# Performance work log

Hardware: AMD Instinct MI355X
Metric: run time of the kernel (lower is better)

The kernel has to match this reference:

```python
import jax, jax.numpy as jnp
import numpy as np

B, S, DM = 1, 2048, 2048
H, KV, DH = 32, 8, 64
ROT, DQ = 32, 16  # rotary dims; DQ = ROT // 2
GROUPS = H // KV


def setup_inputs() -> dict:
    key = jax.random.key(0)
    ks = jax.random.split(key, 9)
    sc = 0.02
    hidden_states = jax.random.normal(ks[0], (B, S, DM), jnp.float32)
    # realistic RoPE tables: theta = pos * inv_freq, shape [1,1,S,DQ] (broadcasts over heads)
    inv_freq = 1.0 / (10000.0 ** (jnp.arange(DQ, dtype=jnp.float32) / DQ))
    ang = jnp.arange(S, dtype=jnp.float32)[:, None] * inv_freq[None, :]
    cos = jnp.cos(ang)[None, None]
    sin = jnp.sin(ang)[None, None]
    position_ids = jnp.broadcast_to(jnp.arange(S, dtype=jnp.int64 if jax.config.read('jax_enable_x64') else jnp.int32), (B, S))
    Wq = jax.random.normal(ks[1], (DM, H * DH), jnp.float32) * sc
    Wk = jax.random.normal(ks[2], (DM, KV * DH), jnp.float32) * sc
    Wv = jax.random.normal(ks[3], (DM, KV * DH), jnp.float32) * sc
    Wo = jax.random.normal(ks[4], (H * DH, DM), jnp.float32) * sc
    qkv_dim = H * DH + 2 * KV * DH
    tau_Wq = jax.random.normal(ks[5], (qkv_dim, H), jnp.float32) * sc
    tau_Wv = jax.random.normal(ks[6], (qkv_dim, H), jnp.float32) * sc
    tau_alpha = jax.random.normal(ks[7], (H,), jnp.float32)
    return {"hidden_states": hidden_states, "cos": cos, "sin": sin,
            "position_ids": position_ids, "Wq": Wq, "Wk": Wk, "Wv": Wv,
            "Wo": Wo, "tau_Wq": tau_Wq, "tau_Wv": tau_Wv, "tau_alpha": tau_alpha}


def _rope(x, cos, sin):
    # x: [B, h, S, DH]; rotate first ROT dims (half-split real/imag), interleave output
    x_rot, x_pass = x[..., :ROT], x[..., ROT:]
    xr, xi = x_rot[..., :DQ], x_rot[..., DQ:]
    out_r = xr * cos - xi * sin
    out_i = xr * sin + xi * cos
    out = jnp.stack([out_r, out_i], axis=-1).reshape(x.shape[:-1] + (ROT,))
    return jnp.concatenate([out, x_pass], axis=-1)


def reference(hidden_states, cos, sin, position_ids, Wq, Wk, Wv, Wo, tau_Wq, tau_Wv, tau_alpha):
    b, s, _ = hidden_states.shape
    q = hidden_states @ Wq                      # [B,S,H*DH]
    k = hidden_states @ Wk                      # [B,S,KV*DH]
    v = hidden_states @ Wv                      # [B,S,KV*DH]
    # tau gating: gelu(concat qkv) -> tanh projections -> position sigmoid term
    feat = jax.nn.gelu(jnp.concatenate([q, k, v], axis=-1), approximate=False)
    tok_q = jnp.tanh(feat @ tau_Wq).transpose(0, 2, 1)   # [B,H,S]
    tok_v = jnp.tanh(feat @ tau_Wv).transpose(0, 2, 1)   # [B,H,S]
    pos = position_ids.astype(hidden_states.dtype) + 1.0
    tau_pos = 1.0 + (jax.nn.sigmoid(tau_alpha[None, :, None] * jnp.log(pos)[:, None, :]) - 0.5)
    tau_q = (tok_q + tau_pos)[..., None]        # [B,H,S,1]
    tau_v = (tok_v + tau_pos)[..., None]        # [B,H,S,1]
    q = q.reshape(b, s, H, DH).transpose(0, 2, 1, 3) * tau_q   # [B,H,S,DH]
    k = k.reshape(b, s, KV, DH).transpose(0, 2, 1, 3)          # [B,KV,S,DH]
    # torch: tau_v.repeat(1,groups,1,1)[:, :KV] == first KV heads of tau_v
    v = v.reshape(b, s, KV, DH).transpose(0, 2, 1, 3) * tau_v[:, :KV]
    q = _rope(q, cos, sin)
    k = _rope(k, cos, sin)
    # GQA expand kv heads, causal SDPA
    k = jnp.repeat(k, GROUPS, axis=1)
    v = jnp.repeat(v, GROUPS, axis=1)
    scores = jnp.einsum('bhqd,bhkd->bhqk', q, k) / np.sqrt(DH).astype(np.float32)
    causal = jnp.tril(jnp.ones((s, s), dtype=bool))
    scores = jnp.where(causal, scores, jnp.finfo(scores.dtype).min)
    attn = jax.nn.softmax(scores, axis=-1)
    out = jnp.einsum('bhqk,bhkd->bhqd', attn, v)
    out = out.transpose(0, 2, 1, 3).reshape(b, s, H * DH)
    return out @ Wo
```

## Files before the change

kernel.cpp:

```cpp
#include <hip/hip_runtime.h>
#include <cmath>

typedef __bf16 bf16x8 __attribute__((ext_vector_type(8)));
typedef __bf16 bf16x4 __attribute__((ext_vector_type(4)));
typedef float f32x4 __attribute__((ext_vector_type(4)));
typedef short s16x4 __attribute__((ext_vector_type(4)));
typedef unsigned short u16;
typedef unsigned int u32;

__device__ __forceinline__ u16 f2bf(float f) {
  union { float f; unsigned int u; } v; v.f = f;
  unsigned int u = v.u;
  return (u16)((u + 0x7FFFu + ((u >> 16) & 1u)) >> 16);
}

__device__ __forceinline__ float bf2f(u16 b) {
  union { u32 u; float f; } v; v.u = (u32)b << 16; return v.f;
}

__device__ __forceinline__ float geluf(float x) {
  return 0.5f * x * (1.0f + erff(x * 0.7071067811865475f));
}

__device__ __forceinline__ f32x4 mfma_16x16x16_bf16(s16x4 a, s16x4 b, f32x4 c) {
#if __has_builtin(__builtin_amdgcn_mfma_f32_16x16x16bf16_1k)
  return __builtin_amdgcn_mfma_f32_16x16x16bf16_1k(a, b, c, 0, 0, 0);
#else
  f32x4 d;
  asm volatile("v_mfma_f32_16x16x16_bf16 %0, %1, %2, %3"
               : "=v"(d) : "v"(a), "v"(b), "0"(c));
  return d;
#endif
}

__device__ __forceinline__ void gl_lds16(const void* g, void* l) {
  __builtin_amdgcn_global_load_lds(
      (const __attribute__((address_space(1))) u32*)g,
      (__attribute__((address_space(3))) u32*)l, 16, 0, 0);
}

__global__ __launch_bounds__(256) void cvt_bf16(const float* __restrict__ in,
                                                u16* __restrict__ out, int n8) {
  int i = blockIdx.x * 256 + threadIdx.x;
  if (i >= n8) return;
  const float4* p = (const float4*)in + 2 * (size_t)i;
  float4 a = p[0], b = p[1];
  uint4 o;
  o.x = (unsigned)f2bf(a.x) | ((unsigned)f2bf(a.y) << 16);
  o.y = (unsigned)f2bf(a.z) | ((unsigned)f2bf(a.w) << 16);
  o.z = (unsigned)f2bf(b.x) | ((unsigned)f2bf(b.y) << 16);
  o.w = (unsigned)f2bf(b.z) | ((unsigned)f2bf(b.w) << 16);
  ((uint4*)out)[i] = o;
}

__global__ __launch_bounds__(256) void transpose_all(const float* __restrict__ Wq,
                                                     const float* __restrict__ Wk,
                                                     const float* __restrict__ Wv,
                                                     const float* __restrict__ Wo,
                                                     const float* __restrict__ tWq,
                                                     const float* __restrict__ tWv,
                                                     u16* __restrict__ WqkvT,
                                                     u16* __restrict__ WoT,
                                                     u16* __restrict__ Tt) {
  __shared__ float tile[64][65];
  int b = blockIdx.x;
  const float* in; u16* out; int R, C, bx, by;
  if (b < 1024)      { in = Wq;  out = WqkvT;                R = 2048; C = 2048; bx = b & 31; by = b >> 5; }
  else if (b < 1280) { b -= 1024; in = Wk; out = WqkvT + 2048ull * 2048; R = 2048; C = 512; bx = b & 7; by = b >> 3; }
  else if (b < 1536) { b -= 1280; in = Wv; out = WqkvT + 2560ull * 2048; R = 2048; C = 512; bx = b & 7; by = b >> 3; }
  else if (b < 2560) { b -= 1536; in = Wo; out = WoT;        R = 2048; C = 2048; bx = b & 31; by = b >> 5; }
  else if (b < 2608) { b -= 2560; in = tWq; out = Tt;               R = 3072; C = 32; bx = 0; by = b; }
  else               { b -= 2608; in = tWv; out = Tt + 32ull * 3072; R = 3072; C = 32; bx = 0; by = b; }

  const int t = threadIdx.x;
  const int r0 = by * 64, c0 = bx * 64;
  const int lr = t >> 4, lc4 = (t & 15) * 4;
#pragma unroll
  for (int p = 0; p < 4; ++p) {
    int r = p * 16 + lr;
    float4 v = {0.f, 0.f, 0.f, 0.f};
    if (c0 + lc4 < C) v = *(const float4*)(in + (size_t)(r0 + r) * C + c0 + lc4);
    tile[r][lc4] = v.x; tile[r][lc4 + 1] = v.y;
    tile[r][lc4 + 2] = v.z; tile[r][lc4 + 3] = v.w;
  }
  __syncthreads();
  const int cg = t >> 4, rr4 = (t & 15) * 4;
#pragma unroll
  for (int p = 0; p < 4; ++p) {
    int c = p * 16 + cg;
    if (c0 + c < C) {
      uint2 w;
      w.x = (u32)f2bf(tile[rr4][c])     | ((u32)f2bf(tile[rr4 + 1][c]) << 16);
      w.y = (u32)f2bf(tile[rr4 + 2][c]) | ((u32)f2bf(tile[rr4 + 3][c]) << 16);
      *(uint2*)(out + (size_t)(c0 + c) * R + r0 + rr4) = w;
    }
  }
}

template <int WR, int WC>
__global__ __launch_bounds__(256, 3) void gemm_bt(const u16* __restrict__ A,
                                                  const u16* __restrict__ Bt,
                                                  float* __restrict__ Cpart,
                                                  int M, int N, int K, int kPer) {
  constexpr int BM = WR * 64, BN = WC * 64;
  __shared__ __attribute__((aligned(16))) u16 As[BM * 64];
  __shared__ __attribute__((aligned(16))) u16 Bs[BN * 64];
  const int tid = threadIdx.x, wid = tid >> 6, lane = tid & 63;
  const int l16 = lane & 15, quad = lane >> 4;
  const int wm = (wid % WR) * 64, wn = (wid / WR) * 64;
  const int m0 = blockIdx.y * BM, n0 = blockIdx.x * BN;
  const int kIters = K >> 6;
  const int kStart = blockIdx.z * kPer;
  const int kEnd = (kStart + kPer < kIters) ? (kStart + kPer) : kIters;

  const int lrow = lane >> 3;
  const int swz = (lane & 7) ^ lrow;
  const u16* gAb = A + (size_t)m0 * K + (size_t)swz * 8;
  const u16* gBb = Bt + (size_t)n0 * K + (size_t)swz * 8;
  const int sx = l16 & 7;

  f32x4 acc[4][4] = {};
  for (int kt = kStart; kt < kEnd; ++kt) {
    __syncthreads();
    const u16* gA = gAb + (size_t)kt * 64;
    const u16* gB = gBb + (size_t)kt * 64;
#pragma unroll
    for (int j = 0; j < BM / 32; ++j) {
      int i = wid * (BM / 32) + j;
      gl_lds16(gA + (size_t)(i * 8 + lrow) * K, &As[i * 512]);
    }
#pragma unroll
    for (int j = 0; j < BN / 32; ++j) {
      int i = wid * (BN / 32) + j;
      gl_lds16(gB + (size_t)(i * 8 + lrow) * K, &Bs[i * 512]);
    }
    __syncthreads();
    bf16x8 af[4][2], bfr[4][2];
#pragma unroll
    for (int mt = 0; mt < 4; ++mt)
#pragma unroll
      for (int ks = 0; ks < 2; ++ks)
        af[mt][ks] = *(const bf16x8*)(&As[(wm + mt * 16 + l16) * 64 +
                                          (((ks * 4 + quad) ^ sx) * 8)]);
#pragma unroll
    for (int nt = 0; nt < 4; ++nt)
#pragma unroll
      for (int ks = 0; ks < 2; ++ks)
        bfr[nt][ks] = *(const bf16x8*)(&Bs[(wn + nt * 16 + l16) * 64 +
                                           (((ks * 4 + quad) ^ sx) * 8)]);
#pragma unroll
    for (int mt = 0; mt < 4; ++mt)
#pragma unroll
      for (int nt = 0; nt < 4; ++nt)
#pragma unroll
        for (int ks = 0; ks < 2; ++ks)
          acc[mt][nt] = __builtin_amdgcn_mfma_f32_16x16x32_bf16(
              af[mt][ks], bfr[nt][ks], acc[mt][nt], 0, 0, 0);
  }

  float* C = Cpart + (size_t)blockIdx.z * M * N;
#pragma unroll
  for (int mt = 0; mt < 4; ++mt)
#pragma unroll
    for (int nt = 0; nt < 4; ++nt)
#pragma unroll
      for (int r = 0; r < 4; ++r) {
        int row = m0 + wm + mt * 16 + quad * 4 + r;
        int col = n0 + wn + nt * 16 + l16;
        C[(size_t)row * N + col] = acc[mt][nt][r];
      }
}

__global__ __launch_bounds__(256) void reduce_gelu(float* __restrict__ base, int P,
                                                   int n4, u16* __restrict__ gout) {
  int i = blockIdx.x * 256 + threadIdx.x;
  if (i >= n4) return;
  size_t n = (size_t)n4 * 4;
  float4 v = ((const float4*)base)[i];
  for (int p = 1; p < P; ++p) {
    float4 w = ((const float4*)(base + (size_t)p * n))[i];
    v.x += w.x; v.y += w.y; v.z += w.z; v.w += w.w;
  }
  if (P > 1) ((float4*)base)[i] = v;
  uint2 o;
  o.x = (u32)f2bf(geluf(v.x)) | ((u32)f2bf(geluf(v.y)) << 16);
  o.y = (u32)f2bf(geluf(v.z)) | ((u32)f2bf(geluf(v.w)) << 16);
  ((uint2*)gout)[i] = o;
}

__global__ __launch_bounds__(256) void reduce_add(const float* __restrict__ base, int P,
                                                  int n4, float* __restrict__ dst) {
  int i = blockIdx.x * 256 + threadIdx.x;
  if (i >= n4) return;
  size_t n = (size_t)n4 * 4;
  float4 v = ((const float4*)base)[i];
  for (int p = 1; p < P; ++p) {
    float4 w = ((const float4*)(base + (size_t)p * n))[i];
    v.x += w.x; v.y += w.y; v.z += w.z; v.w += w.w;
  }
  ((float4*)dst)[i] = v;
}

__global__ __launch_bounds__(256) void reduce_tanh(const float* __restrict__ base, int P,
                                                   int n, float* __restrict__ tokq,
                                                   float* __restrict__ tokv) {
  int i = blockIdx.x * 256 + threadIdx.x;
  if (i >= n) return;
  float v = base[i];
  for (int p = 1; p < P; ++p) v += base[(size_t)p * n + i];
  float t = tanhf(v);
  int col = i & 63, row = i >> 6;
  if (col < 32) tokq[row * 32 + col] = t;
  else          tokv[row * 32 + (col - 32)] = t;
}

#define QSCALE 0.18033688011112042f
__global__ __launch_bounds__(256) void prep_qkv(const float* __restrict__ qkv,
                                                const float* __restrict__ tokq,
                                                const float* __restrict__ tokv,
                                                const float* __restrict__ alpha,
                                                const float* __restrict__ cosb,
                                                const float* __restrict__ sinb,
                                                const int* __restrict__ pos_ids,
                                                u16* __restrict__ Qb,
                                                u16* __restrict__ Kb,
                                                u16* __restrict__ Vt,
                                                u16* __restrict__ Vb) {
  const int s = blockIdx.x;
  const int tid = threadIdx.x;
  __shared__ float cs[16], sn[16], tq_s[32], tv_s[32];
  if (tid < 16) { cs[tid] = cosb[s * 16 + tid]; sn[tid] = sinb[s * 16 + tid]; }
  if (tid < 32) {
    float p = (float)pos_ids[s] + 1.0f;
    float sig = 1.0f / (1.0f + __expf(-alpha[tid] * logf(p)));
    float taupos = 0.5f + sig;
    tq_s[tid] = (tokq[s * 32 + tid] + taupos) * QSCALE;
    tv_s[tid] = tokv[s * 32 + tid] + taupos;
  }
  __syncthreads();
  const float* row = qkv + (size_t)s * 3072;

  for (int idx = tid; idx < 2048; idx += 256) {
    int h = idx >> 6, d = idx & 63;
    float tq = tq_s[h];
    float v;
    if (d < 32) {
      int i = d >> 1;
      float xr = row[h * 64 + i] * tq, xi = row[h * 64 + 16 + i] * tq;
      v = (d & 1) ? (xr * sn[i] + xi * cs[i]) : (xr * cs[i] - xi * sn[i]);
    } else v = row[h * 64 + d] * tq;
    Qb[((size_t)h * 2048 + s) * 64 + d] = f2bf(v);
  }
  for (int idx = tid; idx < 512; idx += 256) {
    int h = idx >> 6, d = idx & 63;
    const float* kr = row + 2048;
    float v;
    if (d < 32) {
      int i = d >> 1;
      float xr = kr[h * 64 + i], xi = kr[h * 64 + 16 + i];
      v = (d & 1) ? (xr * sn[i] + xi * cs[i]) : (xr * cs[i] - xi * sn[i]);
    } else v = kr[h * 64 + d];
    Kb[((size_t)h * 2048 + s) * 64 + d] = f2bf(v);
  }
  for (int idx = tid; idx < 512; idx += 256) {
    int h = idx >> 6, d = idx & 63;
    float v = row[2560 + h * 64 + d] * tv_s[h];
    u16 b = f2bf(v);
    if (Vb) Vb[((size_t)h * 2048 + s) * 64 + d] = b;
    else    Vt[((size_t)h * 64 + d) * 2048 + s] = b;
  }
}

__global__ __launch_bounds__(256) void vtrans(const u16* __restrict__ Vb,
                                              u16* __restrict__ Vt) {
  __shared__ u16 t[64][68];
  const int s0 = blockIdx.x * 64, h = blockIdx.y;
  const int tid = threadIdx.x;
  const u16* src = Vb + ((size_t)h * 2048 + s0) * 64;
#pragma unroll
  for (int p = 0; p < 4; ++p) {
    int v = p * 256 + tid;
    int r = v >> 4, c = (v & 15) * 4;
    uint2 w = *(const uint2*)(src + (size_t)r * 64 + c);
    t[r][c] = (u16)(w.x & 0xffff); t[r][c + 1] = (u16)(w.x >> 16);
    t[r][c + 2] = (u16)(w.y & 0xffff); t[r][c + 3] = (u16)(w.y >> 16);
  }
  __syncthreads();
  u16* dst = Vt + (size_t)h * 64 * 2048 + s0;
#pragma unroll
  for (int p = 0; p < 4; ++p) {
    int v = p * 256 + tid;
    int d = v >> 4, s = (v & 15) * 4;
    uint2 w;
    w.x = (u32)t[s][d] | ((u32)t[s + 1][d] << 16);
    w.y = (u32)t[s + 2][d] | ((u32)t[s + 3][d] << 16);
    *(uint2*)(dst + (size_t)d * 2048 + s) = w;
  }
}

__global__ __launch_bounds__(256, 4) void flash_attn(const u16* __restrict__ Qb,
                                                     const u16* __restrict__ Kb,
                                                     const u16* __restrict__ Vt,
                                                     u16* __restrict__ Opart,
                                                     float* __restrict__ ml) {
  __shared__ __attribute__((aligned(16))) u16 KsB[2][4096];
  __shared__ __attribute__((aligned(16))) u16 VsB[2][4096];
  const int bid = blockIdx.x;
  const int h = (bid & 7) | (((bid >> 3) & 3) << 3);
  const int e = 50 - (bid >> 5);
  const int kvh = h >> 2;
  int a = 0;
  while (3 * (a + 1) * (a + 2) / 2 <= e) ++a;
  const int rem = e - 3 * a * (a + 1) / 2;
  const int qb = 3 * a + rem / (a + 1);
  const int cc = rem % (a + 1);
  const int k0 = cc * 6;
  const int kvTend = 2 * qb + 2;
  const int k1 = (k0 + 6 < kvTend) ? (k0 + 6) : kvTend;
  const int pid = h * 51 + e;

  const int tid = threadIdx.x, wid = tid >> 6, lane = tid & 63;
  const int l16 = lane & 15, quad = lane >> 4;
  const int lrow = lane >> 3, swz = (lane & 7) ^ lrow, sx = l16 & 7;

  const int q0 = qb * 128 + wid * 32;
  bf16x8 qf[2][2];
#pragma unroll
  for (int mt = 0; mt < 2; ++mt)
#pragma unroll
    for (int ks = 0; ks < 2; ++ks)
      qf[mt][ks] = *(const bf16x8*)(Qb + ((size_t)h * 2048 + q0 + mt * 16 + l16) * 64 +
                                    ks * 32 + quad * 8);

  f32x4 oacc[2][4] = {};
  float mrun[2] = {-3e38f, -3e38f};
  float lrun[2] = {0.f, 0.f};

  const u16* kgb = Kb + ((size_t)kvh * 2048) * 64;
  const u16* vgb = Vt + (size_t)kvh * 64 * 2048;

#define FA_STAGE(KT, BUF)                                                         \
  {                                                                               \
    const u16* kg_ = kgb + (size_t)(KT)*64 * 64;                                  \
    const u16* vg_ = vgb + (size_t)(KT)*64;                                       \
    _Pragma("unroll") for (int j = 0; j < 2; ++j) {                               \
      int i_ = wid * 2 + j;                                                       \
      gl_lds16(kg_ + (size_t)(i_ * 8 + lrow) * 64 + swz * 8, &KsB[BUF][i_ * 512]);\
      gl_lds16(vg_ + (size_t)(i_ * 8 + lrow) * 2048 + swz * 8, &VsB[BUF][i_ * 512]);\
    }                                                                             \
  }

  FA_STAGE(k0, 0)
  for (int kt = k0; kt < k1; ++kt) {
    const int cur = (kt - k0) & 1;
    __syncthreads();
    if (kt + 1 < k1) FA_STAGE(kt + 1, cur ^ 1)
    const u16* Ks = KsB[cur];
    const u16* Vs = VsB[cur];

    f32x4 sacc[2][4] = {};
    __builtin_amdgcn_s_setprio(1);
#pragma unroll
    for (int kf = 0; kf < 4; ++kf) {
      bf16x8 a0 = *(const bf16x8*)(Ks + (kf * 16 + l16) * 64 + ((quad ^ sx) << 3));
      bf16x8 a1 = *(const bf16x8*)(Ks + (kf * 16 + l16) * 64 + (((4 + quad) ^ sx) << 3));
      sacc[0][kf] = __builtin_amdgcn_mfma_f32_16x16x32_bf16(a0, qf[0][0], sacc[0][kf], 0, 0, 0);
      sacc[0][kf] = __builtin_amdgcn_mfma_f32_16x16x32_bf16(a1, qf[0][1], sacc[0][kf], 0, 0, 0);
      sacc[1][kf] = __builtin_amdgcn_mfma_f32_16x16x32_bf16(a0, qf[1][0], sacc[1][kf], 0, 0, 0);
      sacc[1][kf] = __builtin_amdgcn_mfma_f32_16x16x32_bf16(a1, qf[1][1], sacc[1][kf], 0, 0, 0);
    }
    __builtin_amdgcn_s_setprio(0);

    const bool msk = (kt >= 2 * qb);
    s16x4 pb[2][4];
#pragma unroll
    for (int mt = 0; mt < 2; ++mt) {
      const int qg = q0 + mt * 16 + l16;
      if (msk) {
        const int kb = kt * 64 + quad * 4;
#pragma unroll
        for (int kf = 0; kf < 4; ++kf)
#pragma unroll
          for (int r = 0; r < 4; ++r)
            if (kb + kf * 16 + r > qg) sacc[mt][kf][r] = -1e9f;
      }
      f32x4 m4 = sacc[mt][0];
      m4 = __builtin_elementwise_max(m4, sacc[mt][1]);
      m4 = __builtin_elementwise_max(m4, sacc[mt][2]);
      m4 = __builtin_elementwise_max(m4, sacc[mt][3]);
      float mx = fmaxf(fmaxf(m4[0], m4[1]), fmaxf(m4[2], m4[3]));
      mx = fmaxf(mx, __shfl_xor(mx, 16));
      mx = fmaxf(mx, __shfl_xor(mx, 32));
      float mn = fmaxf(mrun[mt], mx);
      float al = __builtin_amdgcn_exp2f(mrun[mt] - mn);
      mrun[mt] = mn;
      float psl = 0.f;
#pragma unroll
      for (int kf = 0; kf < 4; ++kf) {
        bf16x4 ph;
#pragma unroll
        for (int r = 0; r < 4; ++r) {
          float p = __builtin_amdgcn_exp2f(sacc[mt][kf][r] - mn);
          psl += p;
          ph[r] = (__bf16)p;
        }
        union { bf16x4 h; s16x4 s; } cv;
        cv.h = ph;
        pb[mt][kf] = cv.s;
      }
      lrun[mt] = lrun[mt] * al + psl;
#pragma unroll
      for (int df = 0; df < 4; ++df) oacc[mt][df] *= al;
    }

    __builtin_amdgcn_s_setprio(1);
#pragma unroll
    for (int kf = 0; kf < 4; ++kf) {
#pragma unroll
      for (int df = 0; df < 4; ++df) {
        s16x4 va = *(const s16x4*)(Vs + (df * 16 + l16) * 64 +
                                   (((kf * 2 + (quad >> 1)) ^ sx) << 3) + ((quad & 1) << 2));
        oacc[0][df] = mfma_16x16x16_bf16(va, pb[0][kf], oacc[0][df]);
        oacc[1][df] = mfma_16x16x16_bf16(va, pb[1][kf], oacc[1][df]);
      }
    }
    __builtin_amdgcn_s_setprio(0);
  }
#undef FA_STAGE

  __syncthreads();
  char* Ls = (char*)KsB;
#pragma unroll
  for (int mt = 0; mt < 2; ++mt) {
    float lt = lrun[mt];
    lt += __shfl_xor(lt, 16);
    lt += __shfl_xor(lt, 32);
    const int qrow = wid * 32 + mt * 16 + l16;
#pragma unroll
    for (int df = 0; df < 4; ++df) {
      uint2 pk2;
      pk2.x = (u32)f2bf(oacc[mt][df][0]) | ((u32)f2bf(oacc[mt][df][1]) << 16);
      pk2.y = (u32)f2bf(oacc[mt][df][2]) | ((u32)f2bf(oacc[mt][df][3]) << 16);
      int boff = qrow * 128 + ((df * 32 + quad * 8) ^ ((qrow & 7) << 4));
      *(uint2*)(Ls + boff) = pk2;
    }
    if (quad == 0) {
      ml[((size_t)pid * 128 + qrow) * 2] = mrun[mt];
      ml[((size_t)pid * 128 + qrow) * 2 + 1] = lt;
    }
  }
  __syncthreads();
  char* Op = (char*)(Opart + (size_t)pid * 128 * 64);
#pragma unroll
  for (int p = 0; p < 4; ++p) {
    int off = p * 4096 + tid * 16;
    int row = off >> 7, wb = off & 127;
    uint4 v = *(const uint4*)(Ls + row * 128 + (wb ^ ((row & 7) << 4)));
    *(uint4*)(Op + off) = v;
  }
}

__global__ __launch_bounds__(256) void fa_combine(const u16* __restrict__ Opart,
                                                  const float* __restrict__ ml,
                                                  u16* __restrict__ Ob) {
  const int qb = blockIdx.x, h = blockIdx.y;
  const int C = (2 * qb + 7) / 6;
  const int aa = qb / 3, bb = qb % 3;
  const int base = h * 51 + 3 * aa * (aa + 1) / 2 + bb * (aa + 1);
  const int t = threadIdx.x;
#pragma unroll
  for (int u = 0; u < 8; ++u) {
    int unit = u * 256 + t;
    int row = unit >> 4, d4 = unit & 15;
    float mstar = -3e38f;
    for (int c = 0; c < C; ++c)
      mstar = fmaxf(mstar, ml[((size_t)(base + c) * 128 + row) * 2]);
    float4 o = {0.f, 0.f, 0.f, 0.f};
    float lsum = 0.f;
    for (int c = 0; c < C; ++c) {
      const float* mlp = &ml[((size_t)(base + c) * 128 + row) * 2];
      float w = __builtin_amdgcn_exp2f(mlp[0] - mstar);
      uint2 v = *(const uint2*)(Opart + ((size_t)(base + c) * 128 + row) * 64 + d4 * 4);
      o.x += w * bf2f((u16)(v.x & 0xffff));
      o.y += w * bf2f((u16)(v.x >> 16));
      o.z += w * bf2f((u16)(v.y & 0xffff));
      o.w += w * bf2f((u16)(v.y >> 16));
      lsum += w * mlp[1];
    }
    float inv = 1.0f / lsum;
    uint2 pk;
    pk.x = (u32)f2bf(o.x * inv) | ((u32)f2bf(o.y * inv) << 16);
    pk.y = (u32)f2bf(o.z * inv) | ((u32)f2bf(o.w * inv) << 16);
    *(uint2*)(Ob + (size_t)(qb * 128 + row) * 2048 + h * 64 + d4 * 4) = pk;
  }
}

extern "C" void kernel_launch(void* const* d_in, const int* in_sizes, int n_in,
                              void* d_out, int out_size, void* d_ws, size_t ws_size,
                              hipStream_t stream) {
  (void)in_sizes; (void)n_in; (void)out_size;
  const float* hidden = (const float*)d_in[0];
  const float* cosb   = (const float*)d_in[1];
  const float* sinb   = (const float*)d_in[2];
  const int*   pos    = (const int*)d_in[3];
  const float* Wq     = (const float*)d_in[4];
  const float* Wk     = (const float*)d_in[5];
  const float* Wv     = (const float*)d_in[6];
  const float* Wo     = (const float*)d_in[7];
  const float* tWq    = (const float*)d_in[8];
  const float* tWv    = (const float*)d_in[9];
  const float* alpha  = (const float*)d_in[10];
  float* out = (float*)d_out;

  const bool big = ws_size >= (size_t)120 * 1024 * 1024;
  const int Pq = big ? 2 : 1;
  const int Pt = big ? 16 : 1;
  const int Po = big ? 2 : 1;

  char* ws = (char*)d_ws;
  size_t off = 0;
  auto alloc = [&](size_t bytes) -> void* {
    void* p = ws + off;
    off += (bytes + 255) & ~(size_t)255;
    return p;
  };
  u16*   WoT   = (u16*)alloc(2048ull * 2048 * 2);
  u16*   Tt    = (u16*)alloc(64ull * 3072 * 2);
  u16*   Qb    = (u16*)alloc(32ull * 2048 * 64 * 2);
  u16*   Kb    = (u16*)alloc(8ull * 2048 * 64 * 2);
  u16*   Vt    = (u16*)alloc(8ull * 64 * 2048 * 2);
  u16*   Ob    = (u16*)alloc(2048ull * 2048 * 2);
  u16*   featb = (u16*)alloc(2048ull * 3072 * 2);
  float* tokq  = (float*)alloc(2048ull * 32 * 4);
  float* tokv  = (float*)alloc(2048ull * 32 * 4);
  u16*   Vb    = big ? (u16*)alloc(8ull * 2048 * 64 * 2) : nullptr;
  size_t E = off;
  u16*   Xb      = (u16*)alloc(2048ull * 2048 * 2);
  u16*   WqkvT   = (u16*)alloc(3072ull * 2048 * 2);
  float* qkvPart = (float*)alloc((size_t)Pq * 2048 * 3072 * 4);
  float* qkv     = qkvPart;
  float* tokPart = (float*)(ws + E);
  u16*   Opart   = (u16*)(ws + E);
  float* mlbuf   = (float*)(ws + E + 1632ull * 128 * 64 * 2);
  float* outPart = (float*)(ws + E);

  cvt_bf16<<<2048, 256, 0, stream>>>(hidden, Xb, 2048 * 2048 / 8);
  transpose_all<<<2656, 256, 0, stream>>>(Wq, Wk, Wv, Wo, tWq, tWv, WqkvT, WoT, Tt);

  gemm_bt<2, 2><<<dim3(24, 16, Pq), 256, 0, stream>>>(
      Xb, WqkvT, qkvPart, 2048, 3072, 2048, (32 + Pq - 1) / Pq);
  reduce_gelu<<<6144, 256, 0, stream>>>(qkvPart, Pq, 2048 * 3072 / 4, featb);

  gemm_bt<4, 1><<<dim3(1, 8, Pt), 256, 0, stream>>>(
      featb, Tt, tokPart, 2048, 64, 3072, (48 + Pt - 1) / Pt);
  reduce_tanh<<<512, 256, 0, stream>>>(tokPart, Pt, 2048 * 64, tokq, tokv);

  prep_qkv<<<2048, 256, 0, stream>>>(qkv, tokq, tokv, alpha, cosb, sinb, pos,
                                     Qb, Kb, Vt, Vb);
  if (big) vtrans<<<dim3(32, 8), 256, 0, stream>>>(Vb, Vt);

  flash_attn<<<1632, 256, 0, stream>>>(Qb, Kb, Vt, Opart, mlbuf);
  fa_combine<<<dim3(16, 32), 256, 0, stream>>>(Opart, mlbuf, Ob);

  gemm_bt<2, 2><<<dim3(16, 16, Po), 256, 0, stream>>>(
      Ob, WoT, outPart, 2048, 2048, 2048, (32 + Po - 1) / Po);
  reduce_add<<<4096, 256, 0, stream>>>(outPart, Po, 2048 * 2048 / 4, out);
}
```

Baseline: 293.1 us.

## Use 8-tile KV chunks and lazy online-softmax rescaling in flash attention

The split-KV work decomposition changes from chunks of up to 6 KV tiles (51 chunks per head) to chunks of up to 8 tiles (40 per head). This cuts the block count and the partial-output traffic in the combine step, but gives each block more sequential work. The online softmax now rescales the accumulators only when the new row max exceeds the running max by more than a threshold (in log2 units), skipping most rescale multiplies at the cost of a wave-wide vote. The row-max and row-sum reductions also gain an extra xor-48 shuffle and are regrouped as a tree.

```diff
diff --git a/kernel.cpp b/kernel.cpp
--- a/kernel.cpp
+++ b/kernel.cpp
@@ -307,17 +307,17 @@
   __shared__ __attribute__((aligned(16))) u16 VsB[2][4096];
   const int bid = blockIdx.x;
   const int h = (bid & 7) | (((bid >> 3) & 3) << 3);
-  const int e = 50 - (bid >> 5);
+  const int e = 39 - (bid >> 5);
   const int kvh = h >> 2;
-  int a = 0;
-  while (3 * (a + 1) * (a + 2) / 2 <= e) ++a;
-  const int rem = e - 3 * a * (a + 1) / 2;
-  const int qb = 3 * a + rem / (a + 1);
-  const int cc = rem % (a + 1);
-  const int k0 = cc * 6;
+  int g = 0;
+  while (2 * (g + 1) * (g + 2) <= e) ++g;
+  const int rem = e - 2 * g * (g + 1);
+  const int qb = 4 * g + rem / (g + 1);
+  const int cc = rem % (g + 1);
+  const int k0 = cc * 8;
   const int kvTend = 2 * qb + 2;
-  const int k1 = (k0 + 6 < kvTend) ? (k0 + 6) : kvTend;
-  const int pid = h * 51 + e;
+  const int k1 = (k0 + 8 < kvTend) ? (k0 + 8) : kvTend;
+  const int pid = h * 40 + e;
 
   const int tid = threadIdx.x, wid = tid >> 6, lane = tid & 63;
   const int l16 = lane & 15, quad = lane >> 4;
@@ -389,11 +389,19 @@
       m4 = __builtin_elementwise_max(m4, sacc[mt][2]);
       m4 = __builtin_elementwise_max(m4, sacc[mt][3]);
       float mx = fmaxf(fmaxf(m4[0], m4[1]), fmaxf(m4[2], m4[3]));
-      mx = fmaxf(mx, __shfl_xor(mx, 16));
-      mx = fmaxf(mx, __shfl_xor(mx, 32));
-      float mn = fmaxf(mrun[mt], mx);
-      float al = __builtin_amdgcn_exp2f(mrun[mt] - mn);
-      mrun[mt] = mn;
+      float x1 = __shfl_xor(mx, 16);
+      float x2 = __shfl_xor(mx, 32);
+      float x3 = __shfl_xor(mx, 48);
+      mx = fmaxf(fmaxf(mx, x1), fmaxf(x2, x3));
+      float mn = mrun[mt];
+      if (!__all(mx <= mrun[mt] + 8.0f)) {
+        mn = fmaxf(mrun[mt], mx);
+        float al = __builtin_amdgcn_exp2f(mrun[mt] - mn);
+        mrun[mt] = mn;
+        lrun[mt] *= al;
+#pragma unroll
+        for (int df = 0; df < 4; ++df) oacc[mt][df] *= al;
+      }
       float psl = 0.f;
 #pragma unroll
       for (int kf = 0; kf < 4; ++kf) {
@@ -408,9 +416,7 @@
         cv.h = ph;
         pb[mt][kf] = cv.s;
       }
-      lrun[mt] = lrun[mt] * al + psl;
-#pragma unroll
-      for (int df = 0; df < 4; ++df) oacc[mt][df] *= al;
+      lrun[mt] += psl;
     }
 
     __builtin_amdgcn_s_setprio(1);
@@ -433,8 +439,10 @@
 #pragma unroll
   for (int mt = 0; mt < 2; ++mt) {
     float lt = lrun[mt];
-    lt += __shfl_xor(lt, 16);
-    lt += __shfl_xor(lt, 32);
+    float a1 = __shfl_xor(lt, 16);
+    float a2 = __shfl_xor(lt, 32);
+    float a3 = __shfl_xor(lt, 48);
+    lt = (lt + a1) + (a2 + a3);
     const int qrow = wid * 32 + mt * 16 + l16;
 #pragma unroll
     for (int df = 0; df < 4; ++df) {
@@ -464,9 +472,9 @@
                                                   const float* __restrict__ ml,
                                                   u16* __restrict__ Ob) {
   const int qb = blockIdx.x, h = blockIdx.y;
-  const int C = (2 * qb + 7) / 6;
-  const int aa = qb / 3, bb = qb % 3;
-  const int base = h * 51 + 3 * aa * (aa + 1) / 2 + bb * (aa + 1);
+  const int g = qb >> 2;
+  const int C = g + 1;
+  const int base = h * 40 + 2 * g * (g + 1) + (qb & 3) * (g + 1);
   const int t = threadIdx.x;
 #pragma unroll
   for (int u = 0; u < 8; ++u) {
@@ -541,7 +549,7 @@
   float* qkv     = qkvPart;
   float* tokPart = (float*)(ws + E);
   u16*   Opart   = (u16*)(ws + E);
-  float* mlbuf   = (float*)(ws + E + 1632ull * 128 * 64 * 2);
+  float* mlbuf   = (float*)(ws + E + 1280ull * 128 * 64 * 2);
   float* outPart = (float*)(ws + E);
 
   cvt_bf16<<<2048, 256, 0, stream>>>(hidden, Xb, 2048 * 2048 / 8);
@@ -559,7 +567,7 @@
                                      Qb, Kb, Vt, Vb);
   if (big) vtrans<<<dim3(32, 8), 256, 0, stream>>>(Vb, Vt);
 
-  flash_attn<<<1632, 256, 0, stream>>>(Qb, Kb, Vt, Opart, mlbuf);
+  flash_attn<<<1280, 256, 0, stream>>>(Qb, Kb, Vt, Opart, mlbuf);
   fa_combine<<<dim3(16, 32), 256, 0, stream>>>(Opart, mlbuf, Ob);
 
   gemm_bt<2, 2><<<dim3(16, 16, Po), 256, 0, stream>>>(
```

Result: faster. 284.9 us (-2.8%).
